# Kernel optimization log

Measured on AMD Instinct MI355X. Metric: run time of the kernel, lower is better.

Reference implementation:

```python
import jax, jax.numpy as jnp
import numpy as np
import math

B, T, C, NH = 8, 1024, 768, 12
HD = C // NH
EPS = 1e-5

def layer_norm(x, g, b):
    mu = jnp.mean(x, axis=-1, keepdims=True)
    var = jnp.mean(jnp.square(x - mu), axis=-1, keepdims=True)
    return (x - mu) * jax.lax.rsqrt(var + EPS) * g + b

def setup_inputs() -> dict:
    key = jax.random.key(0)
    ks = jax.random.split(key, 10)
    s = lambda n: 1.0 / math.sqrt(n)
    return {
        "x": jax.random.normal(ks[0], (B, T, C), jnp.float32),
        "attn_mask": jax.random.randint(ks[1], (B, T), 0, 2, jnp.int32),
        "ln1_g": jnp.ones((C,), jnp.float32),
        "ln1_b": jnp.zeros((C,), jnp.float32),
        "W_attn": jax.random.normal(ks[2], (C, 3 * C), jnp.float32) * s(C),
        "b_attn": jnp.zeros((3 * C,), jnp.float32),
        "W_proj": jax.random.normal(ks[3], (C, C), jnp.float32) * s(C),
        "b_proj": jnp.zeros((C,), jnp.float32),
        "ln2_g": jnp.ones((C,), jnp.float32),
        "ln2_b": jnp.zeros((C,), jnp.float32),
        "W_fc": jax.random.normal(ks[4], (C, 4 * C), jnp.float32) * s(C),
        "b_fc": jnp.zeros((4 * C,), jnp.float32),
        "W_fc2": jax.random.normal(ks[5], (4 * C, C), jnp.float32) * s(4 * C),
        "b_fc2": jnp.zeros((C,), jnp.float32),
    }

def reference(x, attn_mask, ln1_g, ln1_b, W_attn, b_attn, W_proj, b_proj,
              ln2_g, ln2_b, W_fc, b_fc, W_fc2, b_fc2):
    # --- attention branch ---
    h = layer_norm(x, ln1_g, ln1_b)                     # [B,T,C]
    qkv = h @ W_attn + b_attn                           # [B,T,3C]
    q, k, v = jnp.split(qkv, 3, axis=-1)
    q = q.reshape(B, T, NH, HD).transpose(0, 2, 1, 3)   # [B,H,T,D]
    k = k.reshape(B, T, NH, HD).transpose(0, 2, 1, 3)
    v = v.reshape(B, T, NH, HD).transpose(0, 2, 1, 3)
    attn = jnp.einsum('bhqd,bhkd->bhqk', q, k) * (1.0 / math.sqrt(HD))
    mask = attn_mask[:, None, None, :]                  # [B,1,1,T] key-padding
    attn = jnp.where(mask == 0, -jnp.inf, attn)
    attn = jax.nn.softmax(attn, axis=-1)
    o = jnp.einsum('bhqk,bhkd->bhqd', attn, v)          # [B,H,T,D]
    o = o.transpose(0, 2, 1, 3).reshape(B, T, C)
    x = x + (o @ W_proj + b_proj)
    # --- MLP branch ---
    h2 = layer_norm(x, ln2_g, ln2_b)
    h2 = jax.nn.gelu(h2 @ W_fc + b_fc, approximate=True)
    x = x + (h2 @ W_fc2 + b_fc2)
    return x
```

## Files before the change

### kernel.cpp

```cpp
#include <hip/hip_runtime.h>
#include <hip/hip_bf16.h>
#include <math.h>

constexpr int kB  = 8;
constexpr int kT  = 1024;
constexpr int kC  = 768;
constexpr int kNH = 12;
constexpr int kHD = 64;
constexpr int kM  = kB * kT;
constexpr int k3C = 3 * kC;
constexpr int k4C = 4 * kC;

typedef __bf16 bf16x8 __attribute__((ext_vector_type(8)));
typedef float  f32x4  __attribute__((ext_vector_type(4)));
typedef unsigned short u16x8 __attribute__((ext_vector_type(8)));

__device__ inline void gload_lds16(const void* g, void* l) {
  __builtin_amdgcn_global_load_lds(
      (const __attribute__((address_space(1))) void*)g,
      (__attribute__((address_space(3))) void*)l, 16, 0, 0);
}

__global__ __launch_bounds__(256) void ln_kernel(
    const float* __restrict__ x, const float* __restrict__ g,
    const float* __restrict__ bta, __hip_bfloat16* __restrict__ out)
{
  __shared__ float red[4];
  int row = blockIdx.x;
  int tid = threadIdx.x;
  const float* xr = x + (size_t)row * kC;
  float v0 = xr[tid], v1 = xr[tid + 256], v2 = xr[tid + 512];

  float s = v0 + v1 + v2;
#pragma unroll
  for (int off = 32; off; off >>= 1) s += __shfl_xor(s, off);
  if ((tid & 63) == 0) red[tid >> 6] = s;
  __syncthreads();
  float mu = (red[0] + red[1] + red[2] + red[3]) * (1.0f / kC);

  float d0 = v0 - mu, d1 = v1 - mu, d2 = v2 - mu;
  float q = d0 * d0 + d1 * d1 + d2 * d2;
#pragma unroll
  for (int off = 32; off; off >>= 1) q += __shfl_xor(q, off);
  __syncthreads();
  if ((tid & 63) == 0) red[tid >> 6] = q;
  __syncthreads();
  float var = (red[0] + red[1] + red[2] + red[3]) * (1.0f / kC);
  float inv = rsqrtf(var + 1e-5f);

  __hip_bfloat16* orow = out + (size_t)row * kC;
  orow[tid]       = __float2bfloat16(d0 * inv * g[tid]       + bta[tid]);
  orow[tid + 256] = __float2bfloat16(d1 * inv * g[tid + 256] + bta[tid + 256]);
  orow[tid + 512] = __float2bfloat16(d2 * inv * g[tid + 512] + bta[tid + 512]);
}

__global__ __launch_bounds__(256) void transpose_cast(
    const float* __restrict__ W, __hip_bfloat16* __restrict__ WT, int K, int N)
{
  __shared__ __hip_bfloat16 t[64][65];
  int k0 = blockIdx.y * 64, n0 = blockIdx.x * 64;
  int tid = threadIdx.x;
#pragma unroll
  for (int it = 0; it < 16; ++it) {
    int e = it * 256 + tid;
    int r = e >> 6, c = e & 63;
    t[r][c] = __float2bfloat16(W[(size_t)(k0 + r) * N + n0 + c]);
  }
  __syncthreads();
#pragma unroll
  for (int it = 0; it < 16; ++it) {
    int e = it * 256 + tid;
    int nr = e >> 6, kc = e & 63;
    WT[(size_t)(n0 + nr) * K + k0 + kc] = t[kc][nr];
  }
}

__global__ __launch_bounds__(256) void v_transpose(
    const __hip_bfloat16* __restrict__ qkv, __hip_bfloat16* __restrict__ vt)
{
  __shared__ __hip_bfloat16 tile[64][80];
  int b = blockIdx.z, h = blockIdx.y, t0 = blockIdx.x * 64;
  int tid = threadIdx.x;
  const __hip_bfloat16* vb = qkv + (size_t)(b * kT) * k3C + 2 * kC + h * kHD;
#pragma unroll
  for (int it = 0; it < 2; ++it) {
    int e = it * 256 + tid;
    int r = e >> 3, c8 = (e & 7) * 8;
    *(u16x8*)&tile[r][c8] = *(const u16x8*)(vb + (size_t)(t0 + r) * k3C + c8);
  }
  __syncthreads();
  __hip_bfloat16* vrow = vt + (size_t)(b * kNH + h) * kHD * kT;
#pragma unroll
  for (int it = 0; it < 2; ++it) {
    int e = it * 256 + tid;
    int d = e >> 3, k8 = (e & 7) * 8;
    u16x8 u;
#pragma unroll
    for (int m = 0; m < 8; ++m)
      u[m] = *(const unsigned short*)&tile[k8 + m][d];
    *(u16x8*)(vrow + (size_t)d * kT + t0 + k8) = u;
  }
}

__device__ inline float gelu_tanh(float c) {
  float t = 0.7978845608028654f * (c + 0.044715f * c * c * c);
  return 0.5f * c * (1.0f + tanhf(t));
}

template <int OUT_MODE>
__global__ __launch_bounds__(256) void gemm_bf16(
    const __hip_bfloat16* __restrict__ A,
    const __hip_bfloat16* __restrict__ WT,
    const float* __restrict__ bias,
    const float* __restrict__ R,
    void* __restrict__ outv, int M, int N, int K)
{
  __shared__ __align__(16) __hip_bfloat16 sh[2][2][128 * 64];
  const int tid  = threadIdx.x;
  const int lane = tid & 63, wid = tid >> 6;
  const int wr = wid >> 1, wc = wid & 1;
  const int r16 = lane & 15, g = lane >> 4;

  const int nwg = gridDim.x * gridDim.y;
  const int bid = blockIdx.y * gridDim.x + blockIdx.x;
  const int swz = (bid & 7) * (nwg >> 3) + (bid >> 3);
  const int m0 = (swz / gridDim.x) * 128;
  const int n0 = (swz % gridDim.x) * 128;

  const __hip_bfloat16* Abase = A  + (size_t)m0 * K;
  const __hip_bfloat16* Bbase = WT + (size_t)n0 * K;

  f32x4 acc[4][4] = {};

  auto stage = [&](int t) {
    const int buf = t & 1;
    const __hip_bfloat16* As = Abase + t * 64;
    const __hip_bfloat16* Bs = Bbase + t * 64;
#pragma unroll
    for (int it = 0; it < 4; ++it) {
      int e = it * 256 + tid;
      int row = e >> 3, ch = (e & 7) ^ (row & 7);
      char* la = (char*)&sh[buf][0][0] + (it * 4096 + (tid & ~63) * 16);
      char* lb = (char*)&sh[buf][1][0] + (it * 4096 + (tid & ~63) * 16);
      gload_lds16(As + (size_t)row * K + ch * 8, la);
      gload_lds16(Bs + (size_t)row * K + ch * 8, lb);
    }
  };

  const int NT = K >> 6;
  stage(0);
  __syncthreads();

  for (int t = 0; t < NT; ++t) {
    const int buf = t & 1;
    if (t + 1 < NT) stage(t + 1);
    const char* Ab = (const char*)&sh[buf][0][0];
    const char* Bb = (const char*)&sh[buf][1][0];
#pragma unroll
    for (int s = 0; s < 2; ++s) {
      bf16x8 af[4], bf[4];
#pragma unroll
      for (int i = 0; i < 4; ++i) {
        int ar = wr * 64 + i * 16 + r16;
        af[i] = *(const bf16x8*)(Ab + ar * 128 + (((s * 4 + g) ^ (ar & 7)) << 4));
        int br = wc * 64 + i * 16 + r16;
        bf[i] = *(const bf16x8*)(Bb + br * 128 + (((s * 4 + g) ^ (br & 7)) << 4));
      }
#pragma unroll
      for (int i = 0; i < 4; ++i)
#pragma unroll
        for (int j = 0; j < 4; ++j)
          acc[i][j] = __builtin_amdgcn_mfma_f32_16x16x32_bf16(af[i], bf[j],
                                                              acc[i][j], 0, 0, 0);
    }
    __syncthreads();
  }

  const int r0 = m0 + wr * 64 + g * 4;
  const int c0 = n0 + wc * 64 + r16;
#pragma unroll
  for (int i = 0; i < 4; ++i) {
#pragma unroll
    for (int j = 0; j < 4; ++j) {
      int col = c0 + j * 16;
      float bv = bias[col];
#pragma unroll
      for (int q = 0; q < 4; ++q) {
        int row = r0 + i * 16 + q;
        float c = acc[i][j][q] + bv;
        if (OUT_MODE == 1) {
          c += R[(size_t)row * N + col];
          ((float*)outv)[(size_t)row * N + col] = c;
        } else {
          if (OUT_MODE == 2) c = gelu_tanh(c);
          ((__hip_bfloat16*)outv)[(size_t)row * N + col] = __float2bfloat16(c);
        }
      }
    }
  }
}

__global__ __launch_bounds__(256) void attn_mfma(
    const __hip_bfloat16* __restrict__ qkv,
    const __hip_bfloat16* __restrict__ vt,
    const int* __restrict__ mask,
    __hip_bfloat16* __restrict__ o)
{
  __shared__ __align__(16) __hip_bfloat16 Ks[64 * 64];
  __shared__ __align__(16) __hip_bfloat16 Vs[64 * 64];
  __shared__ __align__(16) __hip_bfloat16 Ps[4 * 16 * 64];

  const int b = blockIdx.z, h = blockIdx.y, q0 = blockIdx.x * 64;
  const int tid = threadIdx.x, lane = tid & 63, wid = tid >> 6;
  const int r16 = lane & 15, g = lane >> 4;
  const size_t rs = k3C;
  const __hip_bfloat16* qb = qkv + (size_t)(b * kT) * rs + h * kHD;
  const __hip_bfloat16* kb = qb + kC;
  const __hip_bfloat16* vtb = vt + (size_t)(b * kNH + h) * kHD * kT;
  const int* mrow = mask + b * kT;
  constexpr float kSc = 0.125f * 1.4426950408889634f;

  bf16x8 qf[2];
  {
    const __hip_bfloat16* qr = qb + (size_t)(q0 + wid * 16 + r16) * rs;
#pragma unroll
    for (int s = 0; s < 2; ++s) qf[s] = *(const bf16x8*)(qr + s * 32 + g * 8);
  }

  f32x4 o_acc[4] = {};
  float l_part[4] = {0.f, 0.f, 0.f, 0.f};

  __hip_bfloat16* Pw = Ps + wid * 1024;

  for (int t = 0; t < 16; ++t) {
    __syncthreads();
#pragma unroll
    for (int it = 0; it < 2; ++it) {
      int e = it * 256 + tid;
      int row = e >> 3, ch = (e & 7) ^ (row & 7);
      char* lk = (char*)Ks + (it * 4096 + (tid & ~63) * 16);
      char* lv = (char*)Vs + (it * 4096 + (tid & ~63) * 16);
      gload_lds16(kb + (size_t)(t * 64 + row) * rs + ch * 8, lk);
      gload_lds16(vtb + (size_t)row * kT + t * 64 + ch * 8, lv);
    }
    __syncthreads();

    f32x4 sa[4] = {};
#pragma unroll
    for (int j = 0; j < 4; ++j) {
#pragma unroll
      for (int s = 0; s < 2; ++s) {
        int kr = 16 * j + r16;
        bf16x8 kf = *(const bf16x8*)((const char*)Ks + kr * 128 +
                                     (((s * 4 + g) ^ (kr & 7)) << 4));
        sa[j] = __builtin_amdgcn_mfma_f32_16x16x32_bf16(qf[s], kf, sa[j], 0, 0, 0);
      }
    }

    float keep[4];
#pragma unroll
    for (int j = 0; j < 4; ++j)
      keep[j] = (mrow[t * 64 + 16 * j + r16] != 0) ? 1.f : 0.f;

#pragma unroll
    for (int r = 0; r < 4; ++r) {
      float p[4];
#pragma unroll
      for (int j = 0; j < 4; ++j)
        p[j] = keep[j] != 0.f ? exp2f(sa[j][r] * kSc) : 0.f;
      l_part[r] += (p[0] + p[1]) + (p[2] + p[3]);
      int q = g * 4 + r;
      char* pwq = (char*)Pw + q * 128 + (r16 & 7) * 2;
#pragma unroll
      for (int j = 0; j < 4; ++j) {
        int chn = ((j << 1) | (r16 >> 3)) ^ (q & 7);
        *(__hip_bfloat16*)(pwq + (chn << 4)) = __float2bfloat16(p[j]);
      }
    }

    asm volatile("s_waitcnt lgkmcnt(0)" ::: "memory");
    __builtin_amdgcn_sched_barrier(0);

#pragma unroll
    for (int s = 0; s < 2; ++s) {
      bf16x8 pf = *(const bf16x8*)((const char*)Pw + r16 * 128 +
                                   (((s * 4 + g) ^ (r16 & 7)) << 4));
#pragma unroll
      for (int db = 0; db < 4; ++db) {
        int vr = 16 * db + r16;
        bf16x8 vf = *(const bf16x8*)((const char*)Vs + vr * 128 +
                                     (((s * 4 + g) ^ (vr & 7)) << 4));
        o_acc[db] = __builtin_amdgcn_mfma_f32_16x16x32_bf16(pf, vf, o_acc[db], 0, 0, 0);
      }
    }
  }

#pragma unroll
  for (int r = 0; r < 4; ++r) {
    float l = l_part[r];
#pragma unroll
    for (int off = 8; off; off >>= 1) l += __shfl_xor(l, off);
    float inv = 1.f / l;
    size_t row = (size_t)(b * kT) + q0 + wid * 16 + g * 4 + r;
#pragma unroll
    for (int db = 0; db < 4; ++db)
      o[row * kC + h * kHD + 16 * db + r16] = __float2bfloat16(o_acc[db][r] * inv);
  }
}

extern "C" void kernel_launch(void* const* d_in, const int* in_sizes, int n_in,
                              void* d_out, int out_size, void* d_ws, size_t ws_size,
                              hipStream_t stream) {
  const float* x      = (const float*)d_in[0];
  const int*   amask  = (const int*)  d_in[1];
  const float* ln1_g  = (const float*)d_in[2];
  const float* ln1_b  = (const float*)d_in[3];
  const float* W_attn = (const float*)d_in[4];
  const float* b_attn = (const float*)d_in[5];
  const float* W_proj = (const float*)d_in[6];
  const float* b_proj = (const float*)d_in[7];
  const float* ln2_g  = (const float*)d_in[8];
  const float* ln2_b  = (const float*)d_in[9];
  const float* W_fc   = (const float*)d_in[10];
  const float* b_fc   = (const float*)d_in[11];
  const float* W_fc2  = (const float*)d_in[12];
  const float* b_fc2  = (const float*)d_in[13];
  float* out = (float*)d_out;

  char* ws = (char*)d_ws;
  __hip_bfloat16* h_bf    = (__hip_bfloat16*)(ws);
  __hip_bfloat16* qkv_bf  = (__hip_bfloat16*)(ws + (size_t)16 * 1024 * 1024);
  __hip_bfloat16* fc_bf   = qkv_bf;
  __hip_bfloat16* wt_attn = (__hip_bfloat16*)(ws + (size_t)68 * 1024 * 1024);
  __hip_bfloat16* wt_proj = (__hip_bfloat16*)(ws + (size_t)72 * 1024 * 1024);
  __hip_bfloat16* wt_fc   = (__hip_bfloat16*)(ws + (size_t)74 * 1024 * 1024);
  __hip_bfloat16* wt_fc2  = (__hip_bfloat16*)(ws + (size_t)79 * 1024 * 1024);
  __hip_bfloat16* vt_bf   = (__hip_bfloat16*)(ws + (size_t)84 * 1024 * 1024);

  dim3 blk(256);

  transpose_cast<<<dim3(k3C / 64, kC / 64), blk, 0, stream>>>(W_attn, wt_attn, kC, k3C);
  transpose_cast<<<dim3(kC / 64, kC / 64), blk, 0, stream>>>(W_proj, wt_proj, kC, kC);
  transpose_cast<<<dim3(k4C / 64, kC / 64), blk, 0, stream>>>(W_fc, wt_fc, kC, k4C);
  transpose_cast<<<dim3(kC / 64, k4C / 64), blk, 0, stream>>>(W_fc2, wt_fc2, k4C, kC);

  ln_kernel<<<kM, blk, 0, stream>>>(x, ln1_g, ln1_b, h_bf);
  gemm_bf16<0><<<dim3(k3C / 128, kM / 128), blk, 0, stream>>>(
      h_bf, wt_attn, b_attn, nullptr, qkv_bf, kM, k3C, kC);
  v_transpose<<<dim3(kT / 64, kNH, kB), blk, 0, stream>>>(qkv_bf, vt_bf);
  attn_mfma<<<dim3(kT / 64, kNH, kB), blk, 0, stream>>>(qkv_bf, vt_bf, amask, h_bf);
  gemm_bf16<1><<<dim3(kC / 128, kM / 128), blk, 0, stream>>>(
      h_bf, wt_proj, b_proj, x, out, kM, kC, kC);
  ln_kernel<<<kM, blk, 0, stream>>>(out, ln2_g, ln2_b, h_bf);
  gemm_bf16<2><<<dim3(k4C / 128, kM / 128), blk, 0, stream>>>(
      h_bf, wt_fc, b_fc, nullptr, fc_bf, kM, k4C, kC);
  gemm_bf16<1><<<dim3(kC / 128, kM / 128), blk, 0, stream>>>(
      fc_bf, wt_fc2, b_fc2, out, out, kM, kC, k4C);
}
```

Measured before the change: 267.1 us.

## Add 256x256-tile GEMM kernel with block swizzle for QKV and FC GEMMs

Adds a new bf16 MFMA GEMM kernel with 256x256 output tiles, 512 threads (8 waves each computing 128x64), double-buffered LDS filled by async global-to-LDS loads, and a workgroup-ID swizzle for L2 locality. It is used for the QKV projection and the FC1+GELU GEMMs, which have wide N. The larger tile raises arithmetic intensity and cuts global traffic per FLOP. In exchange it uses 128KB of LDS and many accumulator registers per thread, which limits occupancy and gives fewer workgroups (e.g. 9x32 for QKV), which may underfill the CUs.

Result: slower. 286.1 us (+7.1%).

```diff
diff --git a/kernel.cpp b/kernel.cpp
--- a/kernel.cpp
+++ b/kernel.cpp
@@ -195,6 +195,96 @@
           if (OUT_MODE == 2) c = gelu_tanh(c);
           ((__hip_bfloat16*)outv)[(size_t)row * N + col] = __float2bfloat16(c);
         }
+      }
+    }
+  }
+}
+
+template <int OUT_MODE>
+__global__ __launch_bounds__(512, 2) void gemm_bf16_256(
+    const __hip_bfloat16* __restrict__ A,
+    const __hip_bfloat16* __restrict__ WT,
+    const float* __restrict__ bias,
+    void* __restrict__ outv, int M, int N, int K)
+{
+  __shared__ __align__(16) __hip_bfloat16 sh[2][2][256 * 64];
+  const int tid  = threadIdx.x;
+  const int lane = tid & 63, wid = tid >> 6;
+  const int wm = wid >> 2, wn = wid & 3;
+  const int r16 = lane & 15, g = lane >> 4;
+
+  const int nwg = gridDim.x * gridDim.y;
+  const int bid = blockIdx.y * gridDim.x + blockIdx.x;
+  const int swz = (bid & 7) * (nwg >> 3) + (bid >> 3);
+  const int m0 = (swz / gridDim.x) * 256;
+  const int n0 = (swz % gridDim.x) * 256;
+
+  const __hip_bfloat16* Abase = A  + (size_t)m0 * K;
+  const __hip_bfloat16* Bbase = WT + (size_t)n0 * K;
+
+  f32x4 acc[8][4] = {};
+
+  auto stage = [&](int t) {
+    const int buf = t & 1;
+    const __hip_bfloat16* As = Abase + t * 64;
+    const __hip_bfloat16* Bs = Bbase + t * 64;
+#pragma unroll
+    for (int it = 0; it < 4; ++it) {
+      int e = it * 512 + tid;
+      int row = e >> 3, ch = (e & 7) ^ (row & 7);
+      char* la = (char*)&sh[buf][0][0] + (it * 8192 + (tid & ~63) * 16);
+      char* lb = (char*)&sh[buf][1][0] + (it * 8192 + (tid & ~63) * 16);
+      gload_lds16(As + (size_t)row * K + ch * 8, la);
+      gload_lds16(Bs + (size_t)row * K + ch * 8, lb);
+    }
+  };
+
+  const int NT = K >> 6;
+  stage(0);
+  __syncthreads();
+
+  for (int t = 0; t < NT; ++t) {
+    const int buf = t & 1;
+    if (t + 1 < NT) stage(t + 1);
+    const char* Ab = (const char*)&sh[buf][0][0];
+    const char* Bb = (const char*)&sh[buf][1][0];
+#pragma unroll
+    for (int s = 0; s < 2; ++s) {
+      bf16x8 af[8], bf[4];
+#pragma unroll
+      for (int i = 0; i < 8; ++i) {
+        int ar = wm * 128 + i * 16 + r16;
+        af[i] = *(const bf16x8*)(Ab + ar * 128 + (((s * 4 + g) ^ (ar & 7)) << 4));
+      }
+#pragma unroll
+      for (int j = 0; j < 4; ++j) {
+        int br = wn * 64 + j * 16 + r16;
+        bf[j] = *(const bf16x8*)(Bb + br * 128 + (((s * 4 + g) ^ (br & 7)) << 4));
+      }
+#pragma unroll
+      for (int i = 0; i < 8; ++i)
+#pragma unroll
+        for (int j = 0; j < 4; ++j)
+          acc[i][j] = __builtin_amdgcn_mfma_f32_16x16x32_bf16(af[i], bf[j],
+                                                              acc[i][j], 0, 0, 0);
+    }
+    __syncthreads();
+  }
+
+  const int r0 = m0 + wm * 128 + g * 4;
+  const int c0 = n0 + wn * 64 + r16;
+#pragma unroll
+  for (int i = 0; i < 8; ++i) {
+#pragma unroll
+    for (int j = 0; j < 4; ++j) {
+      int col = c0 + j * 16;
+      float bv = bias[col];
+#pragma unroll
+      for (int q = 0; q < 4; ++q) {
+        int row = r0 + i * 16 + q;
+        float c = acc[i][j][q] + bv;
+        if (OUT_MODE == 2) c = gelu_tanh(c);
+        ((__hip_bfloat16*)outv)[(size_t)row * N + col] = __float2bfloat16(c);
       }
     }
   }
@@ -338,6 +428,7 @@
   __hip_bfloat16* vt_bf   = (__hip_bfloat16*)(ws + (size_t)84 * 1024 * 1024);
 
   dim3 blk(256);
+  dim3 blk512(512);
 
   transpose_cast<<<dim3(k3C / 64, kC / 64), blk, 0, stream>>>(W_attn, wt_attn, kC, k3C);
   transpose_cast<<<dim3(kC / 64, kC / 64), blk, 0, stream>>>(W_proj, wt_proj, kC, kC);
@@ -345,15 +436,15 @@
   transpose_cast<<<dim3(kC / 64, k4C / 64), blk, 0, stream>>>(W_fc2, wt_fc2, k4C, kC);
 
   ln_kernel<<<kM, blk, 0, stream>>>(x, ln1_g, ln1_b, h_bf);
-  gemm_bf16<0><<<dim3(k3C / 128, kM / 128), blk, 0, stream>>>(
-      h_bf, wt_attn, b_attn, nullptr, qkv_bf, kM, k3C, kC);
+  gemm_bf16_256<0><<<dim3(k3C / 256, kM / 256), blk512, 0, stream>>>(
+      h_bf, wt_attn, b_attn, qkv_bf, kM, k3C, kC);
   v_transpose<<<dim3(kT / 64, kNH, kB), blk, 0, stream>>>(qkv_bf, vt_bf);
   attn_mfma<<<dim3(kT / 64, kNH, kB), blk, 0, stream>>>(qkv_bf, vt_bf, amask, h_bf);
   gemm_bf16<1><<<dim3(kC / 128, kM / 128), blk, 0, stream>>>(
       h_bf, wt_proj, b_proj, x, out, kM, kC, kC);
   ln_kernel<<<kM, blk, 0, stream>>>(out, ln2_g, ln2_b, h_bf);
-  gemm_bf16<2><<<dim3(k4C / 128, kM / 128), blk, 0, stream>>>(
-      h_bf, wt_fc, b_fc, nullptr, fc_bf, kM, k4C, kC);
+  gemm_bf16_256<2><<<dim3(k4C / 256, kM / 256), blk512, 0, stream>>>(
+      h_bf, wt_fc, b_fc, fc_bf, kM, k4C, kC);
   gemm_bf16<1><<<dim3(kC / 128, kM / 128), blk, 0, stream>>>(
       fc_bf, wt_fc2, b_fc2, out, out, kM, kC, k4C);
 }
```

## Use triple-buffered BK=32 LDS pipeline with explicit vmcnt waits in GEMM

Applied to the files above, without the earlier changes.

The bf16 GEMM moves from a double-buffered K-tile of 64 to a three-stage ring of K-tile 32, prefetching two tiles ahead. A new swizzled LDS layout packs two 32-wide rows per 128-byte line so bank-conflict avoidance still holds. Explicit s_waitcnt vmcnt and a raw s_barrier replace __syncthreads, so each iteration waits only for the oldest tile instead of draining every load. The goal is to hide global-load latency better, at the cost of twice as many barriers per K and less MFMA work between syncs.

Measured after the change: 309.9 us. 1.16x slower.

```diff
diff --git a/kernel.cpp b/kernel.cpp
--- a/kernel.cpp
+++ b/kernel.cpp
@@ -115,7 +115,8 @@
     const float* __restrict__ R,
     void* __restrict__ outv, int M, int N, int K)
 {
-  __shared__ __align__(16) __hip_bfloat16 sh[2][2][128 * 64];
+  __shared__ __align__(16) __hip_bfloat16 As[3][128 * 32];
+  __shared__ __align__(16) __hip_bfloat16 Bs[3][128 * 32];
   const int tid  = threadIdx.x;
   const int lane = tid & 63, wid = tid >> 6;
   const int wr = wid >> 1, wc = wid & 1;
@@ -132,48 +133,67 @@
 
   f32x4 acc[4][4] = {};
 
-  auto stage = [&](int t) {
-    const int buf = t & 1;
-    const __hip_bfloat16* As = Abase + t * 64;
-    const __hip_bfloat16* Bs = Bbase + t * 64;
-#pragma unroll
-    for (int it = 0; it < 4; ++it) {
+  auto stage = [&](int t, int buf) {
+    const __hip_bfloat16* Ap = Abase + t * 32;
+    const __hip_bfloat16* Bp = Bbase + t * 32;
+#pragma unroll
+    for (int it = 0; it < 2; ++it) {
       int e = it * 256 + tid;
-      int row = e >> 3, ch = (e & 7) ^ (row & 7);
-      char* la = (char*)&sh[buf][0][0] + (it * 4096 + (tid & ~63) * 16);
-      char* lb = (char*)&sh[buf][1][0] + (it * 4096 + (tid & ~63) * 16);
-      gload_lds16(As + (size_t)row * K + ch * 8, la);
-      gload_lds16(Bs + (size_t)row * K + ch * 8, lb);
+      int sr = e >> 3, pcu = (e & 7) ^ (sr & 7);
+      int row = sr * 2 + (pcu >> 2), kch = pcu & 3;
+      char* la = (char*)&As[buf][0] + (it * 4096 + (tid & ~63) * 16);
+      gload_lds16(Ap + (size_t)row * K + kch * 8, la);
+    }
+#pragma unroll
+    for (int it = 0; it < 2; ++it) {
+      int e = it * 256 + tid;
+      int sr = e >> 3, pcu = (e & 7) ^ (sr & 7);
+      int row = sr * 2 + (pcu >> 2), kch = pcu & 3;
+      char* lb = (char*)&Bs[buf][0] + (it * 4096 + (tid & ~63) * 16);
+      gload_lds16(Bp + (size_t)row * K + kch * 8, lb);
     }
   };
 
-  const int NT = K >> 6;
-  stage(0);
-  __syncthreads();
-
+  const int NT = K >> 5;
+
+  stage(0, 0);
+  stage(1, 1);
+  asm volatile("s_waitcnt vmcnt(4)" ::: "memory");
+  __builtin_amdgcn_sched_barrier(0);
+  __builtin_amdgcn_s_barrier();
+  __builtin_amdgcn_sched_barrier(0);
+
+  int cur = 0;
   for (int t = 0; t < NT; ++t) {
-    const int buf = t & 1;
-    if (t + 1 < NT) stage(t + 1);
-    const char* Ab = (const char*)&sh[buf][0][0];
-    const char* Bb = (const char*)&sh[buf][1][0];
-#pragma unroll
-    for (int s = 0; s < 2; ++s) {
-      bf16x8 af[4], bf[4];
-#pragma unroll
-      for (int i = 0; i < 4; ++i) {
-        int ar = wr * 64 + i * 16 + r16;
-        af[i] = *(const bf16x8*)(Ab + ar * 128 + (((s * 4 + g) ^ (ar & 7)) << 4));
-        int br = wc * 64 + i * 16 + r16;
-        bf[i] = *(const bf16x8*)(Bb + br * 128 + (((s * 4 + g) ^ (br & 7)) << 4));
-      }
-#pragma unroll
-      for (int i = 0; i < 4; ++i)
-#pragma unroll
-        for (int j = 0; j < 4; ++j)
-          acc[i][j] = __builtin_amdgcn_mfma_f32_16x16x32_bf16(af[i], bf[j],
-                                                              acc[i][j], 0, 0, 0);
-    }
-    __syncthreads();
+    int nxt = cur + 2; if (nxt >= 3) nxt -= 3;
+    const bool pre = (t + 2 < NT);
+    if (pre) stage(t + 2, nxt);
+
+    const char* Ab = (const char*)&As[cur][0];
+    const char* Bb = (const char*)&Bs[cur][0];
+    bf16x8 af[4], bf[4];
+#pragma unroll
+    for (int i = 0; i < 4; ++i) {
+      int ar = wr * 64 + i * 16 + r16;
+      af[i] = *(const bf16x8*)(Ab + (ar >> 1) * 128 +
+                               (((((ar & 1) << 2) | g) ^ ((ar >> 1) & 7)) << 4));
+      int br = wc * 64 + i * 16 + r16;
+      bf[i] = *(const bf16x8*)(Bb + (br >> 1) * 128 +
+                               (((((br & 1) << 2) | g) ^ ((br >> 1) & 7)) << 4));
+    }
+#pragma unroll
+    for (int i = 0; i < 4; ++i)
+#pragma unroll
+      for (int j = 0; j < 4; ++j)
+        acc[i][j] = __builtin_amdgcn_mfma_f32_16x16x32_bf16(af[i], bf[j],
+                                                            acc[i][j], 0, 0, 0);
+
+    if (pre) { asm volatile("s_waitcnt vmcnt(4)" ::: "memory"); }
+    else     { asm volatile("s_waitcnt vmcnt(0)" ::: "memory"); }
+    __builtin_amdgcn_sched_barrier(0);
+    __builtin_amdgcn_s_barrier();
+    __builtin_amdgcn_sched_barrier(0);
+    cur = cur + 1 == 3 ? 0 : cur + 1;
   }
 
   const int r0 = m0 + wr * 64 + g * 4;
```
